# Optimization experiments

Measured on AMD Instinct MI355X. Metric: run time of the kernel, lower is better.

The kernel has to match this reference:

```python
import math
import jax, jax.numpy as jnp
import numpy as np

# static config (mirrors init_kwargs / input_specs)
B, HRV, WRV, CRV = 2, 32, 1024, 64
CB, HB, WB = 256, 200, 200
D, COUT, HEADS, POINTS = 128, 128, 8, 6
DH = D // HEADS
RMAX = 55.0
XMIN, XMAX, YMIN, YMAX = -50.0, 50.0, -50.0, 50.0


def group_norm(x, gamma, beta, groups, eps=1e-5):
    b, h, w, c = x.shape
    xg = x.reshape(b, h, w, groups, c // groups)
    mean = xg.mean(axis=(1, 2, 4), keepdims=True)
    var = xg.var(axis=(1, 2, 4), keepdims=True)
    xg = (xg - mean) * jax.lax.rsqrt(var + eps)
    return xg.reshape(b, h, w, c) * gamma + beta


def fwd(x_rv, bev, pq_w, pq_b, pv_w, pv_b, po_w, po_b, qs_w1, qs_b1, qs_w2, qs_b2,
        rh_w1, rh_b1, rh_g1, rh_be1, rh_w2, rh_g2, rh_be2, rh_w3, rh_b3,
        so_w, so_b, aw_w, aw_b, vp_w, vp_b, op_w, op_b):
    b = x_rv.shape[0]
    nq = HRV * WRV
    az = jnp.linspace(-math.pi, math.pi, WRV + 1)[:-1]  # [Wrv]
    az = jnp.broadcast_to(az[None, None, :], (b, HRV, WRV))
    coord = jnp.stack([jnp.sin(az), jnp.cos(az), jnp.zeros_like(az)], axis=-1)  # [b,H,W,3]
    Q0 = x_rv @ pq_w + pq_b                                  # 1x1 conv as matmul (NHWC)
    Vmap = bev.transpose(0, 2, 3, 1) @ pv_w + pv_b           # [b,HB,WB,D]
    # range head: 1x1 conv -> GN(8) -> GELU -> 3x3 circular conv -> GN(8) -> GELU -> 1x1 conv
    h = jnp.concatenate([x_rv, coord], axis=-1) @ rh_w1 + rh_b1
    h = jax.nn.gelu(group_norm(h, rh_g1, rh_be1, 8), approximate=False)
    hp = jnp.pad(h, ((0, 0), (1, 1), (1, 1), (0, 0)), mode='wrap')  # circular padding
    h = jax.lax.conv_general_dilated(hp, rh_w2, (1, 1), 'VALID',
                                     dimension_numbers=('NHWC', 'HWIO', 'NHWC'))
    h = jax.nn.gelu(group_norm(h, rh_g2, rh_be2, 8), approximate=False)
    rh = h @ rh_w3 + rh_b3                                   # [b,H,W,2]
    mu = jnp.clip(rh[..., 0], 0.0, RMAX)                     # [b,H,W]
    log_sigma = jnp.clip(rh[..., 1:2], -5.0, 3.0)            # [b,H,W,1]
    sigma = jnp.exp(log_sigma)
    x_mu = mu * jnp.cos(az)
    y_mu = mu * jnp.sin(az)
    rx = jnp.clip((x_mu - XMIN) / (XMAX - XMIN), 0.0, 1.0)
    ry = jnp.clip((y_mu - YMIN) / (YMAX - YMIN), 0.0, 1.0)
    ref = jnp.stack([rx, ry], axis=-1).reshape(b, nq, 2)
    sig_feat = jnp.concatenate([log_sigma, 1.0 / (sigma + 1e-6)], axis=-1)
    q = jnp.concatenate([Q0, sig_feat], axis=-1) @ qs_w1 + qs_b1
    q = jax.nn.gelu(q, approximate=False) @ qs_w2 + qs_b2
    query = q.reshape(b, nq, D)
    # ---- MSDA (num_levels = 1) ----
    value = Vmap.reshape(b, HB * WB, D) @ vp_w + vp_b
    vflat = value.reshape(b, HB * WB, HEADS, DH).transpose(0, 2, 1, 3)  # [b,heads,NV,dh]
    offs = (query @ so_w + so_b).reshape(b, nq, HEADS, POINTS, 2)
    attw = jax.nn.softmax((query @ aw_w + aw_b).reshape(b, nq, HEADS, POINTS), axis=-1)
    norm = jnp.array([WB, HB], dtype=query.dtype)            # offset_normalizer = [W, H]
    loc = ref[:, :, None, None, :] + offs / norm             # [b,nq,heads,P,2] in [0,1]
    loc = loc.transpose(0, 2, 1, 3, 4)                       # [b,heads,nq,P,2]
    attw = attw.transpose(0, 2, 1, 3)                        # [b,heads,nq,P]
    # grid_sample bilinear, zero padding, align_corners=False: pix = loc*size - 0.5
    px = loc[..., 0] * WB - 0.5
    py = loc[..., 1] * HB - 0.5
    x0 = jnp.floor(px).astype(jnp.int32)
    y0 = jnp.floor(py).astype(jnp.int32)
    wx = px - x0
    wy = py - y0

    def gather(xi, yi):
        valid = (xi >= 0) & (xi < WB) & (yi >= 0) & (yi < HB)
        idx = jnp.clip(yi, 0, HB - 1) * WB + jnp.clip(xi, 0, WB - 1)
        g = jnp.take_along_axis(vflat, idx.reshape(b, HEADS, nq * POINTS, 1), axis=2)
        return g.reshape(b, HEADS, nq, POINTS, DH) * valid[..., None]

    sampled = (gather(x0, y0) * ((1 - wx) * (1 - wy))[..., None]
               + gather(x0 + 1, y0) * (wx * (1 - wy))[..., None]
               + gather(x0, y0 + 1) * ((1 - wx) * wy)[..., None]
               + gather(x0 + 1, y0 + 1) * (wx * wy)[..., None])    # [b,heads,nq,P,dh]
    out = (sampled * attw[..., None]).sum(axis=3)                  # [b,heads,nq,dh]
    out = out.transpose(0, 2, 1, 3).reshape(b, nq, D) @ op_w + op_b
    y = out.reshape(b, HRV, WRV, D) @ po_w + po_b                  # proj_o (1x1 conv)
    return y                                                       # [b,Hrv,Wrv,C_out]


def setup_inputs() -> dict:
    key = jax.random.key(0)
    ks = jax.random.split(key, 20)
    def rn(i, shape, s=0.02):
        return s * jax.random.normal(ks[i], shape, jnp.float32)
    z = lambda n: jnp.zeros((n,), jnp.float32)
    o = lambda n: jnp.ones((n,), jnp.float32)
    return dict(
        x_rv=rn(0, (B, HRV, WRV, CRV), 1.0),
        bev=rn(1, (B, CB, HB, WB), 1.0),
        pq_w=rn(2, (CRV, D)), pq_b=z(D),
        pv_w=rn(3, (CB, D)), pv_b=z(D),
        po_w=rn(4, (D, COUT)), po_b=z(COUT),
        qs_w1=rn(5, (D + 2, D)), qs_b1=z(D),
        qs_w2=rn(6, (D, D)), qs_b2=z(D),
        rh_w1=rn(7, (CRV + 3, 128)), rh_b1=z(128),
        rh_g1=o(128), rh_be1=z(128),
        rh_w2=rn(8, (3, 3, 128, 64)),
        rh_g2=o(64), rh_be2=z(64),
        rh_w3=rn(9, (64, 2)), rh_b3=z(2),
        so_w=rn(10, (D, HEADS * POINTS * 2)), so_b=rn(11, (HEADS * POINTS * 2,), 0.5),
        aw_w=rn(12, (D, HEADS * POINTS)), aw_b=z(HEADS * POINTS),
        vp_w=rn(13, (D, D)), vp_b=z(D),
        op_w=rn(14, (D, D)), op_b=z(D),
    )


def reference(x_rv, bev, pq_w, pq_b, pv_w, pv_b, po_w, po_b, qs_w1, qs_b1, qs_w2, qs_b2,
              rh_w1, rh_b1, rh_g1, rh_be1, rh_w2, rh_g2, rh_be2, rh_w3, rh_b3,
              so_w, so_b, aw_w, aw_b, vp_w, vp_b, op_w, op_b):
    return fwd(x_rv, bev, pq_w, pq_b, pv_w, pv_b, po_w, po_b, qs_w1, qs_b1, qs_w2, qs_b2,
               rh_w1, rh_b1, rh_g1, rh_be1, rh_w2, rh_g2, rh_be2, rh_w3, rh_b3,
               so_w, so_b, aw_w, aw_b, vp_w, vp_b, op_w, op_b)
```

## Files before the change

### kernel.cpp

```cpp
#include <hip/hip_runtime.h>
#include <math.h>

#define PI_F 3.14159265358979323846f


typedef __attribute__((ext_vector_type(8))) short bf16x8;
typedef __attribute__((ext_vector_type(4))) float f32x4;

__device__ __forceinline__ float gelu_f(float x) {
    return 0.5f * x * (1.0f + erff(x * 0.70710678118654752440f));
}

__device__ __forceinline__ unsigned short f2bf(float x) {
    unsigned int u = __float_as_uint(x);
    u += 0x7fffu + ((u >> 16) & 1u);
    return (unsigned short)(u >> 16);
}

__device__ __forceinline__ float bf2f(unsigned short h) {
    return __uint_as_float((unsigned int)h << 16);
}

__global__ void prep_weights(const float* __restrict__ pv_w, const float* __restrict__ pv_b,
                             const float* __restrict__ vp_w, const float* __restrict__ vp_b,
                             const float* __restrict__ op_w, const float* __restrict__ op_b,
                             const float* __restrict__ po_w, const float* __restrict__ po_b,
                             const float* __restrict__ pq_w, const float* __restrict__ pq_b,
                             const float* __restrict__ qs_w1, const float* __restrict__ qs_b1,
                             const float* __restrict__ qs_w2, const float* __restrict__ qs_b2,
                             const float* __restrict__ so_w, const float* __restrict__ so_b,
                             const float* __restrict__ aw_w, const float* __restrict__ aw_b,
                             const float* __restrict__ rh_w2,
                             unsigned short* __restrict__ wvh, unsigned short* __restrict__ wvl,
                             float* __restrict__ pvvp_b,
                             float* __restrict__ oppo_w, float* __restrict__ oppo_b,
                             float* __restrict__ pqqs_w, float* __restrict__ pqqs_b,
                             float* __restrict__ qsso_w, float* __restrict__ qsso_b,
                             float* __restrict__ qsaw_w, float* __restrict__ qsaw_b,
                             unsigned short* __restrict__ wtb,
                             float2* __restrict__ azsc) {
    int r = blockIdx.x;
    int d = threadIdx.x;
    if (r < 256) {
        float s = 0.f;
        for (int k = 0; k < 128; ++k) s += pv_w[r * 128 + k] * vp_w[k * 128 + d];
        unsigned short h = f2bf(s);
        wvh[d * 256 + r] = h;
        wvl[d * 256 + r] = f2bf(s - bf2f(h));
    } else if (r == 256) {
        float s = vp_b[d];
        for (int k = 0; k < 128; ++k) s += pv_b[k] * vp_w[k * 128 + d];
        pvvp_b[d] = s;
    } else if (r < 385) {
        int rr = r - 257;
        float s = 0.f;
        for (int k = 0; k < 128; ++k) s += op_w[rr * 128 + k] * po_w[k * 128 + d];
        oppo_w[rr * 128 + d] = s;
    } else if (r == 385) {
        float s = po_b[d];
        for (int k = 0; k < 128; ++k) s += op_b[k] * po_w[k * 128 + d];
        oppo_b[d] = s;
    } else if (r < 450) {
        int rr = r - 386;
        float s = 0.f;
        for (int k = 0; k < 128; ++k) s += pq_w[rr * 128 + k] * qs_w1[k * 128 + d];
        pqqs_w[rr * 128 + d] = s;
    } else if (r == 450) {
        float s = qs_b1[d];
        for (int k = 0; k < 128; ++k) s += pq_b[k] * qs_w1[k * 128 + d];
        pqqs_b[d] = s;
    } else if (r < 459) {
        int w = (r - 451) * 128 + d;
        float az = -PI_F + (float)w * (6.283185307179586f / 1024.0f);
        azsc[w] = make_float2(sinf(az), cosf(az));
    } else if (r < 587) {
        int rr = r - 459;
        if (d < 96) {
            float s = 0.f;
            for (int k = 0; k < 128; ++k) s += qs_w2[rr * 128 + k] * so_w[k * 96 + d];
            qsso_w[rr * 96 + d] = s;
        }
    } else if (r == 587) {
        if (d < 96) {
            float s = so_b[d];
            for (int k = 0; k < 128; ++k) s += qs_b2[k] * so_w[k * 96 + d];
            qsso_b[d] = s;
        }
    } else if (r < 716) {
        int rr = r - 588;
        if (d < 48) {
            float s = 0.f;
            for (int k = 0; k < 128; ++k) s += qs_w2[rr * 128 + k] * aw_w[k * 48 + d];
            qsaw_w[rr * 48 + d] = s;
        }
    } else if (r == 716) {
        if (d < 48) {
            float s = aw_b[d];
            for (int k = 0; k < 128; ++k) s += qs_b2[k] * aw_w[k * 48 + d];
            qsaw_b[d] = s;
        }
    } else {
        int idx = (r - 717) * 128 + d;
        int ci = idx & 31;
        int o = (idx >> 5) & 63;
        int cc4i = (idx >> 11) & 3;
        int tap = idx >> 13;
        float w = rh_w2[((size_t)tap * 128 + cc4i * 32 + ci) * 64 + o];
        wtb[idx] = f2bf(w);
    }
}

template <int NT, bool STATS>
__global__ __launch_bounds__(2 * NT) void gemm_v3(
    const float* __restrict__ A, int lda,
    const float* __restrict__ W,
    const float* __restrict__ bias,
    float* __restrict__ C, int K,
    const float2* __restrict__ azsc,
    const float* __restrict__ extra2,
    const float* __restrict__ extra_w,
    int emode, int do_gelu, float* __restrict__ stats1) {
    constexpr int NTH = 2 * NT;
    constexpr int NTO = NT / 8;
    __shared__ float As[32][140];
    __shared__ float Ws[32][NT];
    __shared__ float sred[8][2];
    const int tid = threadIdx.x;
    const int tn = tid % NTO;
    const int tm = tid / NTO;
    const int m0 = blockIdx.x * 128;
    if (STATS && tid < 16) sred[tid >> 1][tid & 1] = 0.f;
    float acc[8][8];
#pragma unroll
    for (int i = 0; i < 8; ++i)
#pragma unroll
        for (int j = 0; j < 8; ++j) acc[i][j] = 0.f;

    for (int k0 = 0; k0 < K; k0 += 32) {
        __syncthreads();
        for (int f = tid; f < 1024; f += NTH) {
            int r = f >> 3, c4 = f & 7;
            float4 v = *(const float4*)(A + (size_t)(m0 + r) * lda + k0 + c4 * 4);
            As[c4 * 4 + 0][r] = v.x;
            As[c4 * 4 + 1][r] = v.y;
            As[c4 * 4 + 2][r] = v.z;
            As[c4 * 4 + 3][r] = v.w;
        }
        for (int f = tid; f < 8 * NT; f += NTH) {
            int kk = f / (NT / 4), n4 = f % (NT / 4);
            *(float4*)&Ws[kk][n4 * 4] = *(const float4*)(W + (size_t)(k0 + kk) * NT + n4 * 4);
        }
        __syncthreads();
#pragma unroll 2
        for (int k = 0; k < 32; ++k) {
            const float4 a0 = *(const float4*)&As[k][tm * 8];
            const float4 a1 = *(const float4*)&As[k][tm * 8 + 4];
            const float4 w0 = *(const float4*)&Ws[k][tn * 8];
            const float4 w1 = *(const float4*)&Ws[k][tn * 8 + 4];
            const float av[8] = {a0.x, a0.y, a0.z, a0.w, a1.x, a1.y, a1.z, a1.w};
            const float wv[8] = {w0.x, w0.y, w0.z, w0.w, w1.x, w1.y, w1.z, w1.w};
#pragma unroll
            for (int i = 0; i < 8; ++i)
#pragma unroll
                for (int j = 0; j < 8; ++j) acc[i][j] += av[i] * wv[j];
        }
    }
    float bv[8], e0w[8], e1w[8];
#pragma unroll
    for (int j = 0; j < 8; ++j) bv[j] = bias[tn * 8 + j];
    if (emode) {
#pragma unroll
        for (int j = 0; j < 8; ++j) {
            e0w[j] = extra_w[tn * 8 + j];
            e1w[j] = extra_w[NT + tn * 8 + j];
        }
    }
    float ts = 0.f, ts2 = 0.f;
#pragma unroll
    for (int i = 0; i < 8; ++i) {
        int m = m0 + tm * 8 + i;
        float e0 = 0.f, e1 = 0.f;
        if (emode == 1) {
            float2 sc = azsc[m & 1023];
            e0 = sc.x; e1 = sc.y;
        } else if (emode == 2) {
            e0 = extra2[2 * (size_t)m];
            e1 = extra2[2 * (size_t)m + 1];
        }
        float o[8];
#pragma unroll
        for (int j = 0; j < 8; ++j) {
            float v = acc[i][j] + bv[j];
            if (emode) v += e0 * e0w[j] + e1 * e1w[j];
            if (do_gelu) v = gelu_f(v);
            if (STATS) { ts += v; ts2 += v * v; }
            o[j] = v;
        }
        *(float4*)(C + (size_t)m * NT + tn * 8) = make_float4(o[0], o[1], o[2], o[3]);
        *(float4*)(C + (size_t)m * NT + tn * 8 + 4) = make_float4(o[4], o[5], o[6], o[7]);
    }
    if (STATS) {
        atomicAdd(&sred[tn >> 1][0], ts);
        atomicAdd(&sred[tn >> 1][1], ts2);
        __syncthreads();
        if (tid < 8) {
            int b = m0 >> 15;
            atomicAdd(&stats1[(b * 8 + tid) * 2 + 0], sred[tid][0]);
            atomicAdd(&stats1[(b * 8 + tid) * 2 + 1], sred[tid][1]);
        }
    }
}

template <int MT, int NT, int NTH>
__global__ __launch_bounds__(NTH) void gemm_rn(
    const float* __restrict__ A, int lda,
    const float* __restrict__ W, int ldw,
    const float* __restrict__ bias,
    float* __restrict__ C, int ldc, int K) {
    static_assert(NTH == (MT / 8) * (NT / 4), "thread count mismatch");
    __shared__ float As[32][MT + 12];
    __shared__ float Ws[32][NT];
    constexpr int NTN = NT / 4;
    const int tid = threadIdx.x;
    const int tn = tid % NTN;
    const int tm = tid / NTN;
    const int m0 = blockIdx.x * MT;
    float acc[8][4];
#pragma unroll
    for (int i = 0; i < 8; ++i)
#pragma unroll
        for (int j = 0; j < 4; ++j) acc[i][j] = 0.f;

    for (int k0 = 0; k0 < K; k0 += 32) {
        __syncthreads();
        for (int f = tid; f < MT * 8; f += NTH) {
            int r = f >> 3, c4 = f & 7;
            float4 v = *(const float4*)(A + (size_t)(m0 + r) * lda + k0 + c4 * 4);
            As[c4 * 4 + 0][r] = v.x;
            As[c4 * 4 + 1][r] = v.y;
            As[c4 * 4 + 2][r] = v.z;
            As[c4 * 4 + 3][r] = v.w;
        }
        for (int f = tid; f < 8 * NT; f += NTH) {
            int kk = f / NTN, n4 = f % NTN;
            *(float4*)&Ws[kk][n4 * 4] = *(const float4*)(W + (size_t)(k0 + kk) * ldw + n4 * 4);
        }
        __syncthreads();
#pragma unroll 4
        for (int k = 0; k < 32; ++k) {
            const float4 a0 = *(const float4*)&As[k][tm * 8];
            const float4 a1 = *(const float4*)&As[k][tm * 8 + 4];
            const float4 wv = *(const float4*)&Ws[k][tn * 4];
            acc[0][0] += a0.x * wv.x; acc[0][1] += a0.x * wv.y; acc[0][2] += a0.x * wv.z; acc[0][3] += a0.x * wv.w;
            acc[1][0] += a0.y * wv.x; acc[1][1] += a0.y * wv.y; acc[1][2] += a0.y * wv.z; acc[1][3] += a0.y * wv.w;
            acc[2][0] += a0.z * wv.x; acc[2][1] += a0.z * wv.y; acc[2][2] += a0.z * wv.z; acc[2][3] += a0.z * wv.w;
            acc[3][0] += a0.w * wv.x; acc[3][1] += a0.w * wv.y; acc[3][2] += a0.w * wv.z; acc[3][3] += a0.w * wv.w;
            acc[4][0] += a1.x * wv.x; acc[4][1] += a1.x * wv.y; acc[4][2] += a1.x * wv.z; acc[4][3] += a1.x * wv.w;
            acc[5][0] += a1.y * wv.x; acc[5][1] += a1.y * wv.y; acc[5][2] += a1.y * wv.z; acc[5][3] += a1.y * wv.w;
            acc[6][0] += a1.z * wv.x; acc[6][1] += a1.z * wv.y; acc[6][2] += a1.z * wv.z; acc[6][3] += a1.z * wv.w;
            acc[7][0] += a1.w * wv.x; acc[7][1] += a1.w * wv.y; acc[7][2] += a1.w * wv.z; acc[7][3] += a1.w * wv.w;
        }
    }
#pragma unroll
    for (int i = 0; i < 8; ++i) {
        int m = m0 + tm * 8 + i;
        float4 o;
        o.x = acc[i][0] + bias[tn * 4 + 0];
        o.y = acc[i][1] + bias[tn * 4 + 1];
        o.z = acc[i][2] + bias[tn * 4 + 2];
        o.w = acc[i][3] + bias[tn * 4 + 3];
        *(float4*)(C + (size_t)m * ldc + tn * 4) = o;
    }
}

__global__ __launch_bounds__(256) void value_gemm_mfma(
    const float* __restrict__ bev,
    const unsigned short* __restrict__ Wh, const unsigned short* __restrict__ Wl,
    const float* __restrict__ bf, float* __restrict__ V) {
    __shared__ __align__(16) short Ah0_s[64 * 40];
    __shared__ __align__(16) short Al0_s[64 * 40];
    __shared__ __align__(16) short Ah1_s[64 * 40];
    __shared__ __align__(16) short Al1_s[64 * 40];
    const int tid = threadIdx.x;
    const int wid = tid >> 6;
    const int lane = tid & 63;
    const int m = lane & 15;
    const int quad = lane >> 4;
    const int n0 = blockIdx.x * 64;
    const int b = blockIdx.y;
    const int wr = (wid >> 1) * 32;
    const int wc = (wid & 1) * 64;
    f32x4 acc[2][4];
#pragma unroll
    for (int i = 0; i < 2; ++i)
#pragma unroll
        for (int j = 0; j < 4; ++j) acc[i][j] = (f32x4){0.f, 0.f, 0.f, 0.f};

    const int sn = tid & 63;
    const int kq = tid >> 6;
    const float* srcA = bev + (size_t)b * 256 * 40000 + n0 + sn;
    const unsigned short* pBh[4];
    const unsigned short* pBl[4];
#pragma unroll
    for (int j = 0; j < 4; ++j) {
        size_t off = (size_t)(wc + j * 16 + m) * 256 + quad * 8;
        pBh[j] = Wh + off;
        pBl[j] = Wl + off;
    }

    float va[8];
    bf16x8 vbh[4], vbl[4];
#pragma unroll
    for (int j = 0; j < 8; ++j) va[j] = srcA[(size_t)(kq * 8 + j) * 40000];
#pragma unroll
    for (int j = 0; j < 4; ++j) {
        vbh[j] = *(const bf16x8*)(pBh[j]);
        vbl[j] = *(const bf16x8*)(pBl[j]);
    }

    short* pAh = Ah0_s; short* pAl = Al0_s;
    short* qAh = Ah1_s; short* qAl = Al1_s;

    for (int t = 0; t < 8; ++t) {
        const int k0 = t * 32;
        uint4 ph, pl;
        {
            unsigned hp[4], lp[4];
#pragma unroll
            for (int pj = 0; pj < 4; ++pj) {
                float x0 = va[2 * pj], x1 = va[2 * pj + 1];
                unsigned u0 = __float_as_uint(x0), u1 = __float_as_uint(x1);
                hp[pj] = __builtin_amdgcn_perm(u1, u0, 0x07060302);
                float h0 = __uint_as_float(u0 & 0xffff0000u);
                float h1 = __uint_as_float(u1 & 0xffff0000u);
                float l0 = x0 - h0, l1 = x1 - h1;
                asm("v_cvt_pk_bf16_f32 %0, %1, %2" : "=v"(lp[pj]) : "v"(l0), "v"(l1));
            }
            ph = make_uint4(hp[0], hp[1], hp[2], hp[3]);
            pl = make_uint4(lp[0], lp[1], lp[2], lp[3]);
        }
        *(uint4*)&pAh[sn * 40 + kq * 8] = ph;
        *(uint4*)&pAl[sn * 40 + kq * 8] = pl;
        if (t < 7) {
#pragma unroll
            for (int j = 0; j < 8; ++j)
                va[j] = srcA[(size_t)(k0 + 32 + kq * 8 + j) * 40000];
        }
        asm volatile("s_waitcnt lgkmcnt(0)" ::: "memory");
        __builtin_amdgcn_sched_barrier(0);
        __builtin_amdgcn_s_barrier();
        __builtin_amdgcn_sched_barrier(0);
        bf16x8 ah[2], al[2];
#pragma unroll
        for (int i = 0; i < 2; ++i) {
            ah[i] = *(const bf16x8*)&pAh[(wr + i * 16 + m) * 40 + quad * 8];
            al[i] = *(const bf16x8*)&pAl[(wr + i * 16 + m) * 40 + quad * 8];
        }
#pragma unroll
        for (int i = 0; i < 2; ++i)
#pragma unroll
            for (int j = 0; j < 4; ++j) {
                acc[i][j] = __builtin_amdgcn_mfma_f32_16x16x32_bf16(ah[i], vbh[j], acc[i][j], 0, 0, 0);
                acc[i][j] = __builtin_amdgcn_mfma_f32_16x16x32_bf16(ah[i], vbl[j], acc[i][j], 0, 0, 0);
                acc[i][j] = __builtin_amdgcn_mfma_f32_16x16x32_bf16(al[i], vbh[j], acc[i][j], 0, 0, 0);
            }
        if (t < 7) {
#pragma unroll
            for (int j = 0; j < 4; ++j) {
                vbh[j] = *(const bf16x8*)(pBh[j] + k0 + 32);
                vbl[j] = *(const bf16x8*)(pBl[j] + k0 + 32);
            }
        }
        short* th = pAh; pAh = qAh; qAh = th;
        short* tl = pAl; pAl = qAl; qAl = tl;
    }
    float bv[4];
#pragma unroll
    for (int j = 0; j < 4; ++j) bv[j] = bf[wc + j * 16 + m];
#pragma unroll
    for (int i = 0; i < 2; ++i) {
        int nbase = n0 + wr + i * 16 + quad * 4;
#pragma unroll
        for (int r = 0; r < 4; ++r) {
            int n = nbase + r;
            float* vp = V + ((size_t)b * 40000 + n) * 128 + wc + m;
#pragma unroll
            for (int j = 0; j < 4; ++j) vp[j * 16] = acc[i][j][r] + bv[j];
        }
    }
}

__global__ __launch_bounds__(256) void gn1_bf16(
    const float* __restrict__ X, const float* __restrict__ stats,
    const float* __restrict__ g1, const float* __restrict__ be1,
    unsigned short* __restrict__ Ob) {
    size_t i4 = (size_t)blockIdx.x * 256 + threadIdx.x;
    size_t base = i4 * 4;
    int c = (int)(base & 127);
    int mrow = (int)(base >> 7);
    int b = mrow >> 15;
    int g = c >> 4;
    float mean = stats[(b * 8 + g) * 2 + 0] * (1.0f / 524288.0f);
    float var = stats[(b * 8 + g) * 2 + 1] * (1.0f / 524288.0f) - mean * mean;
    float rs = 1.0f / sqrtf(var + 1e-5f);
    float4 x = *(const float4*)(X + base);
    float4 gm = *(const float4*)(g1 + c);
    float4 bt = *(const float4*)(be1 + c);
    ushort4 o;
    o.x = f2bf(gelu_f((x.x - mean) * rs * gm.x + bt.x));
    o.y = f2bf(gelu_f((x.y - mean) * rs * gm.y + bt.y));
    o.z = f2bf(gelu_f((x.z - mean) * rs * gm.z + bt.z));
    o.w = f2bf(gelu_f((x.w - mean) * rs * gm.w + bt.w));
    *(ushort4*)(Ob + base) = o;
}

__global__ __launch_bounds__(256, 4) void conv3x3_mfma(
    const unsigned short* __restrict__ H1b,
    const unsigned short* __restrict__ Wtb,
    float* __restrict__ Y,
    float* __restrict__ stats2) {
    __shared__ short As_s[66 * 40];
    __shared__ short Ws_s[3 * 64 * 40];
    __shared__ float sred[8][2];
    const int tid = threadIdx.x;
    const int wid = tid >> 6;
    const int lane = tid & 63;
    const int m = lane & 15;
    const int quad = lane >> 4;
    const int x0 = blockIdx.x * 64;
    const int y = blockIdx.y;
    const int b = blockIdx.z;
    if (tid < 16) sred[tid >> 1][tid & 1] = 0.f;
    f32x4 acc[4];
#pragma unroll
    for (int oq = 0; oq < 4; ++oq) acc[oq] = (f32x4){0.f, 0.f, 0.f, 0.f};

    const unsigned short* Hb = H1b + (size_t)b * 32 * 1024 * 128;
    for (int ry = 0; ry < 3; ++ry) {
        const int gy = (y + ry + 31) & 31;
        const unsigned short* Hrow = Hb + (size_t)gy * 1024 * 128;
        for (int cc4 = 0; cc4 < 4; ++cc4) {
            __syncthreads();
            for (int f = tid; f < 264; f += 256) {
                int xx = f >> 2, cq = f & 3;
                int gx = (x0 + xx + 1023) & 1023;
                uint4 v = *(const uint4*)(Hrow + (size_t)gx * 128 + cc4 * 32 + cq * 8);
                *(uint4*)&As_s[xx * 40 + cq * 8] = v;
            }
            for (int f = tid; f < 768; f += 256) {
                int cq = f & 3, o = (f >> 2) & 63, dx = f >> 8;
                int tap = ry * 3 + dx;
                uint4 v = *(const uint4*)(Wtb + ((size_t)(tap * 4 + cc4) * 64 + o) * 32 + cq * 8);
                *(uint4*)&Ws_s[(dx * 64 + o) * 40 + cq * 8] = v;
            }
            __syncthreads();
            const int arow = wid * 16 + m;
#pragma unroll
            for (int dx = 0; dx < 3; ++dx) {
                bf16x8 a = *(const bf16x8*)&As_s[(arow + dx) * 40 + quad * 8];
#pragma unroll
                for (int oq = 0; oq < 4; ++oq) {
                    bf16x8 bfr = *(const bf16x8*)&Ws_s[(dx * 64 + oq * 16 + m) * 40 + quad * 8];
                    acc[oq] = __builtin_amdgcn_mfma_f32_16x16x32_bf16(a, bfr, acc[oq], 0, 0, 0);
                }
            }
        }
    }
    float sv[4], qv[4];
#pragma unroll
    for (int oq = 0; oq < 4; ++oq) {
        sv[oq] = acc[oq].x + acc[oq].y + acc[oq].z + acc[oq].w;
        qv[oq] = acc[oq].x * acc[oq].x + acc[oq].y * acc[oq].y +
                 acc[oq].z * acc[oq].z + acc[oq].w * acc[oq].w;
    }
    const int masks[5] = {1, 2, 4, 16, 32};
#pragma unroll
    for (int mi = 0; mi < 5; ++mi) {
#pragma unroll
        for (int oq = 0; oq < 4; ++oq) {
            sv[oq] += __shfl_xor(sv[oq], masks[mi]);
            qv[oq] += __shfl_xor(qv[oq], masks[mi]);
        }
    }
    if ((lane & 55) == 0) {
        int gb = (lane >> 3) & 1;
#pragma unroll
        for (int oq = 0; oq < 4; ++oq) {
            atomicAdd(&sred[oq * 2 + gb][0], sv[oq]);
            atomicAdd(&sred[oq * 2 + gb][1], qv[oq]);
        }
    }
    const int pxb = x0 + wid * 16 + quad * 4;
    float* Yb = Y + ((size_t)(b * 32 + y) * 1024 + pxb) * 64;
#pragma unroll
    for (int oq = 0; oq < 4; ++oq) {
        const float av[4] = {acc[oq].x, acc[oq].y, acc[oq].z, acc[oq].w};
#pragma unroll
        for (int r = 0; r < 4; ++r) Yb[(size_t)r * 64 + oq * 16 + m] = av[r];
    }
    __syncthreads();
    if (tid < 16)
        atomicAdd(&stats2[(b * 8 + (tid >> 1)) * 2 + (tid & 1)], sred[tid >> 1][tid & 1]);
}

__global__ __launch_bounds__(256) void rh3_kernel(
    const float* __restrict__ H2, const float* __restrict__ stats,
    const float* __restrict__ gamma, const float* __restrict__ beta, float inv_cnt,
    const float* __restrict__ w3, const float* __restrict__ b3,
    const float2* __restrict__ azsc,
    float2* __restrict__ refxy, float2* __restrict__ sigf) {
    const int tid = threadIdx.x;
    const int lane = tid & 15;
    const int m = blockIdx.x * 16 + (tid >> 4);
    const int b = m >> 15;
    const int c = lane * 4;
    const int g = c >> 3;
    float mean = stats[(b * 8 + g) * 2 + 0] * inv_cnt;
    float var = stats[(b * 8 + g) * 2 + 1] * inv_cnt - mean * mean;
    float rs = 1.0f / sqrtf(var + 1e-5f);
    float4 v = *(const float4*)(H2 + (size_t)m * 64 + c);
    float hv[4];
    hv[0] = gelu_f((v.x - mean) * rs * gamma[c + 0] + beta[c + 0]);
    hv[1] = gelu_f((v.y - mean) * rs * gamma[c + 1] + beta[c + 1]);
    hv[2] = gelu_f((v.z - mean) * rs * gamma[c + 2] + beta[c + 2]);
    hv[3] = gelu_f((v.w - mean) * rs * gamma[c + 3] + beta[c + 3]);
    float d0 = 0.f, d1 = 0.f;
#pragma unroll
    for (int k = 0; k < 4; ++k) {
        d0 += hv[k] * w3[(c + k) * 2 + 0];
        d1 += hv[k] * w3[(c + k) * 2 + 1];
    }
#pragma unroll
    for (int s = 1; s < 16; s <<= 1) {
        d0 += __shfl_xor(d0, s, 16);
        d1 += __shfl_xor(d1, s, 16);
    }
    if (lane == 0) {
        float mu = fminf(fmaxf(d0 + b3[0], 0.f), 55.f);
        float ls = fminf(fmaxf(d1 + b3[1], -5.f), 3.f);
        float sg = expf(ls);
        float2 sc = azsc[m & 1023];
        float rx = fminf(fmaxf(mu * sc.y * 0.01f + 0.5f, 0.f), 1.f);
        float ry = fminf(fmaxf(mu * sc.x * 0.01f + 0.5f, 0.f), 1.f);
        refxy[m] = make_float2(rx, ry);
        sigf[m] = make_float2(ls, 1.f / (sg + 1e-6f));
    }
}

__global__ __launch_bounds__(256) void msda_kernel(
    const float* __restrict__ V, const float2* __restrict__ refxy,
    const float* __restrict__ offs, const float* __restrict__ aw,
    float* __restrict__ out) {
    const int tid = threadIdx.x;
    const int l4 = tid & 3;
    const int grp = tid >> 2;
    const int m = blockIdx.x * 8 + (grp >> 3);
    const int head = grp & 7;
    const int b = m >> 15;
    float2 r = refxy[m];
    const float* lg = aw + (size_t)m * 48 + head * 6;
    float l[6];
#pragma unroll
    for (int p = 0; p < 6; ++p) l[p] = lg[p];
    float mx = l[0];
#pragma unroll
    for (int p = 1; p < 6; ++p) mx = fmaxf(mx, l[p]);
    float s = 0.f;
#pragma unroll
    for (int p = 0; p < 6; ++p) { l[p] = expf(l[p] - mx); s += l[p]; }
    float inv = 1.f / s;
#pragma unroll
    for (int p = 0; p < 6; ++p) l[p] *= inv;
    const float* of = offs + (size_t)m * 96 + head * 12;
    const float* Vb = V + (size_t)b * 40000 * 128 + head * 16 + l4 * 4;
    const float bx = r.x * 200.f - 0.5f;
    const float by = r.y * 200.f - 0.5f;
    f32x4 acc = (f32x4){0.f, 0.f, 0.f, 0.f};
#pragma unroll
    for (int p = 0; p < 6; ++p) {
        float px = bx + of[p * 2 + 0];
        float py = by + of[p * 2 + 1];
        float fx = floorf(px), fy = floorf(py);
        int x0 = (int)fx, y0 = (int)fy;
        float wx = px - fx, wy = py - fy;
        int xc0 = min(max(x0, 0), 199), xc1 = min(max(x0 + 1, 0), 199);
        int yc0 = min(max(y0, 0), 199), yc1 = min(max(y0 + 1, 0), 199);
        bool vx0 = ((unsigned)x0 < 200u), vx1 = ((unsigned)(x0 + 1) < 200u);
        bool vy0 = ((unsigned)y0 < 200u), vy1 = ((unsigned)(y0 + 1) < 200u);
        const f32x4 v00 = *(const f32x4*)(Vb + ((size_t)(yc0 * 200 + xc0)) * 128);
        const f32x4 v10 = *(const f32x4*)(Vb + ((size_t)(yc0 * 200 + xc1)) * 128);
        const f32x4 v01 = *(const f32x4*)(Vb + ((size_t)(yc1 * 200 + xc0)) * 128);
        const f32x4 v11 = *(const f32x4*)(Vb + ((size_t)(yc1 * 200 + xc1)) * 128);
        float w = l[p];
        float w00 = (vx0 && vy0) ? w * (1.f - wx) * (1.f - wy) : 0.f;
        float w10 = (vx1 && vy0) ? w * wx * (1.f - wy) : 0.f;
        float w01 = (vx0 && vy1) ? w * (1.f - wx) * wy : 0.f;
        float w11 = (vx1 && vy1) ? w * wx * wy : 0.f;
        acc += v00 * w00;
        acc += v10 * w10;
        acc += v01 * w01;
        acc += v11 * w11;
    }
    *(f32x4*)(out + (size_t)m * 128 + head * 16 + l4 * 4) = acc;
}

extern "C" void kernel_launch(void* const* d_in, const int* in_sizes, int n_in,
                              void* d_out, int out_size, void* d_ws, size_t ws_size,
                              hipStream_t stream) {
    const float* x_rv = (const float*)d_in[0];
    const float* bev = (const float*)d_in[1];
    const float* pq_w = (const float*)d_in[2];
    const float* pq_b = (const float*)d_in[3];
    const float* pv_w = (const float*)d_in[4];
    const float* pv_b = (const float*)d_in[5];
    const float* po_w = (const float*)d_in[6];
    const float* po_b = (const float*)d_in[7];
    const float* qs_w1 = (const float*)d_in[8];
    const float* qs_b1 = (const float*)d_in[9];
    const float* qs_w2 = (const float*)d_in[10];
    const float* qs_b2 = (const float*)d_in[11];
    const float* rh_w1 = (const float*)d_in[12];
    const float* rh_b1 = (const float*)d_in[13];
    const float* rh_g1 = (const float*)d_in[14];
    const float* rh_be1 = (const float*)d_in[15];
    const float* rh_w2 = (const float*)d_in[16];
    const float* rh_g2 = (const float*)d_in[17];
    const float* rh_be2 = (const float*)d_in[18];
    const float* rh_w3 = (const float*)d_in[19];
    const float* rh_b3 = (const float*)d_in[20];
    const float* so_w = (const float*)d_in[21];
    const float* so_b = (const float*)d_in[22];
    const float* aw_w = (const float*)d_in[23];
    const float* aw_b = (const float*)d_in[24];
    const float* vp_w = (const float*)d_in[25];
    const float* vp_b = (const float*)d_in[26];
    const float* op_w = (const float*)d_in[27];
    const float* op_b = (const float*)d_in[28];

    const int M = 65536;

    float* ws = (float*)d_ws;
    float* azsc = ws;    ws += 2048;
    unsigned short* wvh = (unsigned short*)ws; ws += 16384;
    unsigned short* wvl = (unsigned short*)ws; ws += 16384;
    float* pvvp_b = ws;  ws += 128;
    float* oppo_w = ws;  ws += 128 * 128;
    float* oppo_b = ws;  ws += 128;
    float* pqqs_w = ws;  ws += 64 * 128;
    float* pqqs_b = ws;  ws += 128;
    float* qsso_w = ws;  ws += 128 * 96;
    float* qsso_b = ws;  ws += 128;
    float* qsaw_w = ws;  ws += 128 * 48;
    float* qsaw_b = ws;  ws += 64;
    float* stats = ws;   ws += 64;
    unsigned short* wtb = (unsigned short*)ws;  ws += 36864;
    unsigned short* h1b = (unsigned short*)ws;  ws += (size_t)M * 64;
    float* Vv = ws;      ws += (size_t)80000 * 128;
    float* h1 = ws;      ws += (size_t)M * 128;
    float* h2 = ws;      ws += (size_t)M * 64;
    float* q1 = ws;      ws += (size_t)M * 128;
    float* refxy = ws;   ws += (size_t)M * 2;
    float* sigf = ws;    ws += (size_t)M * 2;
    size_t need_bytes = (size_t)(ws - (float*)d_ws) * sizeof(float);
    if (ws_size < need_bytes) return;
    float* offs = h1;
    float* attw = h2;
    float* mo = q1;

    float2* azsc2 = (float2*)azsc;
    float2* refxy2 = (float2*)refxy;
    float2* sigf2 = (float2*)sigf;

    prep_weights<<<1293, 128, 0, stream>>>(
        pv_w, pv_b, vp_w, vp_b, op_w, op_b, po_w, po_b, pq_w, pq_b,
        qs_w1, qs_b1, qs_w2, qs_b2, so_w, so_b, aw_w, aw_b, rh_w2,
        wvh, wvl, pvvp_b, oppo_w, oppo_b, pqqs_w, pqqs_b,
        qsso_w, qsso_b, qsaw_w, qsaw_b, wtb, azsc2);
    hipMemsetAsync(stats, 0, 64 * sizeof(float), stream);

    gemm_v3<128, true><<<M / 128, 256, 0, stream>>>(
        x_rv, 64, rh_w1, rh_b1, h1, 64, azsc2, nullptr, rh_w1 + 64 * 128, 1, 0, stats);

    value_gemm_mfma<<<dim3(625, 2), 256, 0, stream>>>(bev, wvh, wvl, pvvp_b, Vv);

    gn1_bf16<<<8192, 256, 0, stream>>>(h1, stats, rh_g1, rh_be1, h1b);

    conv3x3_mfma<<<dim3(16, 32, 2), 256, 0, stream>>>(h1b, wtb, h2, stats + 32);

    rh3_kernel<<<4096, 256, 0, stream>>>(h2, stats + 32, rh_g2, rh_be2, 1.0f / 262144.0f,
                                         rh_w3, rh_b3, azsc2, refxy2, sigf2);

    gemm_v3<128, false><<<M / 128, 256, 0, stream>>>(
        x_rv, 64, pqqs_w, pqqs_b, q1, 64, nullptr, sigf, qs_w1 + 128 * 128, 2, 1, nullptr);

    gemm_v3<96, false><<<M / 128, 192, 0, stream>>>(
        q1, 128, qsso_w, qsso_b, offs, 128, nullptr, nullptr, nullptr, 0, 0, nullptr);

    gemm_rn<128, 48, 192><<<M / 128, 192, 0, stream>>>(
        q1, 128, qsaw_w, 48, qsaw_b, attw, 48, 128);

    msda_kernel<<<M / 8, 256, 0, stream>>>(Vv, refxy2, offs, attw, mo);

    gemm_v3<128, false><<<M / 128, 256, 0, stream>>>(
        mo, 128, oppo_w, oppo_b, (float*)d_out, 128, nullptr, nullptr, nullptr, 0, 0, nullptr);
}
```

Baseline: 486.2 us.

## Restructure BEV value GEMM with float4 staging and pre-swizzled weight layout

The value-projection GEMM now stages raw fp32 BEV tiles in LDS with coalesced float4 global loads and does the bf16 hi/lo split at fragment-read time, replacing per-thread strided scalar loads. Weights are pre-swizzled in prep_weights so each lane reads its MFMA B fragment contiguously, and these fragments are loaded directly from global memory every K step. Blocks grow to 512 threads covering 128 pixels, with a clamped tail and guarded stores. The kernel is also launched before the range-head GEMM. In exchange there are more LDS reads and conversions per wave, and weight loads are no longer prefetched one step ahead.

Result: faster. 469.6 us (-3.4%).

```diff
diff --git a/kernel.cpp b/kernel.cpp
--- a/kernel.cpp
+++ b/kernel.cpp
@@ -45,8 +45,11 @@
         float s = 0.f;
         for (int k = 0; k < 128; ++k) s += pv_w[r * 128 + k] * vp_w[k * 128 + d];
         unsigned short h = f2bf(s);
-        wvh[d * 256 + r] = h;
-        wvl[d * 256 + r] = f2bf(s - bf2f(h));
+        int dt = d >> 4, mm = d & 15;
+        int kc = r >> 5, qd = (r >> 3) & 3, jj = r & 7;
+        size_t off = (((size_t)(dt * 8 + kc) * 64) + qd * 16 + mm) * 8 + jj;
+        wvh[off] = h;
+        wvl[off] = f2bf(s - bf2f(h));
     } else if (r == 256) {
         float s = vp_b[d];
         for (int k = 0; k < 128; ++k) s += pv_b[k] * vp_w[k * 128 + d];
@@ -273,119 +276,141 @@
     }
 }
 
-__global__ __launch_bounds__(256) void value_gemm_mfma(
+__global__ __launch_bounds__(512) void value_gemm_fused(
     const float* __restrict__ bev,
     const unsigned short* __restrict__ Wh, const unsigned short* __restrict__ Wl,
     const float* __restrict__ bf, float* __restrict__ V) {
-    __shared__ __align__(16) short Ah0_s[64 * 40];
-    __shared__ __align__(16) short Al0_s[64 * 40];
-    __shared__ __align__(16) short Ah1_s[64 * 40];
-    __shared__ __align__(16) short Al1_s[64 * 40];
+    __shared__ __align__(16) float T0[32 * 134];
+    __shared__ __align__(16) float T1[32 * 134];
     const int tid = threadIdx.x;
     const int wid = tid >> 6;
     const int lane = tid & 63;
     const int m = lane & 15;
     const int quad = lane >> 4;
-    const int n0 = blockIdx.x * 64;
+    const int n0 = blockIdx.x * 128;
     const int b = blockIdx.y;
-    const int wr = (wid >> 1) * 32;
-    const int wc = (wid & 1) * 64;
+    const int wn = wid >> 1;
+    const int wd = wid & 1;
+    const float* src = bev + (size_t)b * 256 * 40000;
+
+    int srow[2];
+    const float* sp[2];
+    int lcol[2];
+#pragma unroll
+    for (int i = 0; i < 2; ++i) {
+        int f = tid + i * 512;
+        srow[i] = f >> 5;
+        lcol[i] = (f & 31) * 4;
+        int nl = n0 + lcol[i];
+        if (nl > 39996) nl = 39996;
+        sp[i] = src + nl;
+    }
+
     f32x4 acc[2][4];
 #pragma unroll
     for (int i = 0; i < 2; ++i)
 #pragma unroll
         for (int j = 0; j < 4; ++j) acc[i][j] = (f32x4){0.f, 0.f, 0.f, 0.f};
 
-    const int sn = tid & 63;
-    const int kq = tid >> 6;
-    const float* srcA = bev + (size_t)b * 256 * 40000 + n0 + sn;
-    const unsigned short* pBh[4];
-    const unsigned short* pBl[4];
-#pragma unroll
-    for (int j = 0; j < 4; ++j) {
-        size_t off = (size_t)(wc + j * 16 + m) * 256 + quad * 8;
-        pBh[j] = Wh + off;
-        pBl[j] = Wl + off;
-    }
-
-    float va[8];
-    bf16x8 vbh[4], vbl[4];
-#pragma unroll
-    for (int j = 0; j < 8; ++j) va[j] = srcA[(size_t)(kq * 8 + j) * 40000];
-#pragma unroll
-    for (int j = 0; j < 4; ++j) {
-        vbh[j] = *(const bf16x8*)(pBh[j]);
-        vbl[j] = *(const bf16x8*)(pBl[j]);
-    }
-
-    short* pAh = Ah0_s; short* pAl = Al0_s;
-    short* qAh = Ah1_s; short* qAl = Al1_s;
+    const int dt0 = wd * 4;
+    size_t bb[4];
+#pragma unroll
+    for (int j = 0; j < 4; ++j) bb[j] = (size_t)(dt0 + j) * 4096 + lane * 8;
+
+    union UV { uint4 u; bf16x8 v; };
+    float4 st[2];
+
+#define LOADG(K0)                                                           \
+    {                                                                       \
+        _Pragma("unroll")                                                   \
+        for (int i_ = 0; i_ < 2; ++i_)                                      \
+            st[i_] = *(const float4*)(sp[i_] + (size_t)((K0) + srow[i_]) * 40000); \
+    }
+#define WRITELDS(TB)                                                        \
+    {                                                                       \
+        _Pragma("unroll")                                                   \
+        for (int i_ = 0; i_ < 2; ++i_) {                                    \
+            float* d_ = (TB) + srow[i_] * 134 + lcol[i_];                   \
+            *(float2*)(d_ + 0) = make_float2(st[i_].x, st[i_].y);           \
+            *(float2*)(d_ + 2) = make_float2(st[i_].z, st[i_].w);           \
+        }                                                                   \
+    }
+
+    float* Tc = T0;
+    float* Tn = T1;
+    LOADG(0);
+    WRITELDS(Tc);
+    LOADG(32);
+    asm volatile("s_waitcnt lgkmcnt(0)" ::: "memory");
+    __builtin_amdgcn_sched_barrier(0);
+    __builtin_amdgcn_s_barrier();
+    __builtin_amdgcn_sched_barrier(0);
 
     for (int t = 0; t < 8; ++t) {
-        const int k0 = t * 32;
-        uint4 ph, pl;
-        {
-            unsigned hp[4], lp[4];
-#pragma unroll
-            for (int pj = 0; pj < 4; ++pj) {
-                float x0 = va[2 * pj], x1 = va[2 * pj + 1];
-                unsigned u0 = __float_as_uint(x0), u1 = __float_as_uint(x1);
-                hp[pj] = __builtin_amdgcn_perm(u1, u0, 0x07060302);
-                float h0 = __uint_as_float(u0 & 0xffff0000u);
-                float h1 = __uint_as_float(u1 & 0xffff0000u);
-                float l0 = x0 - h0, l1 = x1 - h1;
-                asm("v_cvt_pk_bf16_f32 %0, %1, %2" : "=v"(lp[pj]) : "v"(l0), "v"(l1));
+        bf16x8 ah[2], al[2];
+#pragma unroll
+        for (int i = 0; i < 2; ++i) {
+            const int nc = wn * 32 + i * 16 + m;
+            float f8[8];
+#pragma unroll
+            for (int jj = 0; jj < 8; ++jj)
+                f8[jj] = Tc[(quad * 8 + jj) * 134 + nc];
+            unsigned hh[4], ll[4];
+#pragma unroll
+            for (int q = 0; q < 4; ++q) {
+                unsigned u0 = __float_as_uint(f8[2 * q]);
+                unsigned u1 = __float_as_uint(f8[2 * q + 1]);
+                hh[q] = __builtin_amdgcn_perm(u1, u0, 0x07060302);
+                float l0 = f8[2 * q] - __uint_as_float(u0 & 0xffff0000u);
+                float l1 = f8[2 * q + 1] - __uint_as_float(u1 & 0xffff0000u);
+                asm("v_cvt_pk_bf16_f32 %0, %1, %2" : "=v"(ll[q]) : "v"(l0), "v"(l1));
             }
-            ph = make_uint4(hp[0], hp[1], hp[2], hp[3]);
-            pl = make_uint4(lp[0], lp[1], lp[2], lp[3]);
-        }
-        *(uint4*)&pAh[sn * 40 + kq * 8] = ph;
-        *(uint4*)&pAl[sn * 40 + kq * 8] = pl;
-        if (t < 7) {
-#pragma unroll
-            for (int j = 0; j < 8; ++j)
-                va[j] = srcA[(size_t)(k0 + 32 + kq * 8 + j) * 40000];
-        }
-        asm volatile("s_waitcnt lgkmcnt(0)" ::: "memory");
-        __builtin_amdgcn_sched_barrier(0);
-        __builtin_amdgcn_s_barrier();
-        __builtin_amdgcn_sched_barrier(0);
-        bf16x8 ah[2], al[2];
-#pragma unroll
-        for (int i = 0; i < 2; ++i) {
-            ah[i] = *(const bf16x8*)&pAh[(wr + i * 16 + m) * 40 + quad * 8];
-            al[i] = *(const bf16x8*)&pAl[(wr + i * 16 + m) * 40 + quad * 8];
+            UV th, tl;
+            th.u = make_uint4(hh[0], hh[1], hh[2], hh[3]);
+            tl.u = make_uint4(ll[0], ll[1], ll[2], ll[3]);
+            ah[i] = th.v;
+            al[i] = tl.v;
+        }
+        if (t < 7) WRITELDS(Tn);
+        if (t < 6) LOADG(t * 32 + 64);
+        bf16x8 bh[4], bl[4];
+#pragma unroll
+        for (int j = 0; j < 4; ++j) {
+            bh[j] = *(const bf16x8*)(Wh + bb[j] + t * 512);
+            bl[j] = *(const bf16x8*)(Wl + bb[j] + t * 512);
         }
 #pragma unroll
         for (int i = 0; i < 2; ++i)
 #pragma unroll
             for (int j = 0; j < 4; ++j) {
-                acc[i][j] = __builtin_amdgcn_mfma_f32_16x16x32_bf16(ah[i], vbh[j], acc[i][j], 0, 0, 0);
-                acc[i][j] = __builtin_amdgcn_mfma_f32_16x16x32_bf16(ah[i], vbl[j], acc[i][j], 0, 0, 0);
-                acc[i][j] = __builtin_amdgcn_mfma_f32_16x16x32_bf16(al[i], vbh[j], acc[i][j], 0, 0, 0);
+                acc[i][j] = __builtin_amdgcn_mfma_f32_16x16x32_bf16(ah[i], bh[j], acc[i][j], 0, 0, 0);
+                acc[i][j] = __builtin_amdgcn_mfma_f32_16x16x32_bf16(ah[i], bl[j], acc[i][j], 0, 0, 0);
+                acc[i][j] = __builtin_amdgcn_mfma_f32_16x16x32_bf16(al[i], bh[j], acc[i][j], 0, 0, 0);
             }
         if (t < 7) {
-#pragma unroll
-            for (int j = 0; j < 4; ++j) {
-                vbh[j] = *(const bf16x8*)(pBh[j] + k0 + 32);
-                vbl[j] = *(const bf16x8*)(pBl[j] + k0 + 32);
-            }
-        }
-        short* th = pAh; pAh = qAh; qAh = th;
-        short* tl = pAl; pAl = qAl; qAl = tl;
-    }
+            asm volatile("s_waitcnt lgkmcnt(0)" ::: "memory");
+            __builtin_amdgcn_sched_barrier(0);
+            __builtin_amdgcn_s_barrier();
+            __builtin_amdgcn_sched_barrier(0);
+            float* tmp = Tc; Tc = Tn; Tn = tmp;
+        }
+    }
+#undef LOADG
+#undef WRITELDS
     float bv[4];
 #pragma unroll
-    for (int j = 0; j < 4; ++j) bv[j] = bf[wc + j * 16 + m];
+    for (int j = 0; j < 4; ++j) bv[j] = bf[wd * 64 + j * 16 + m];
 #pragma unroll
     for (int i = 0; i < 2; ++i) {
-        int nbase = n0 + wr + i * 16 + quad * 4;
+        int nbase = n0 + wn * 32 + i * 16 + quad * 4;
 #pragma unroll
         for (int r = 0; r < 4; ++r) {
             int n = nbase + r;
-            float* vp = V + ((size_t)b * 40000 + n) * 128 + wc + m;
-#pragma unroll
-            for (int j = 0; j < 4; ++j) vp[j * 16] = acc[i][j][r] + bv[j];
+            if (n < 40000) {
+                float* vp = V + ((size_t)b * 40000 + n) * 128 + wd * 64 + m;
+#pragma unroll
+                for (int j = 0; j < 4; ++j) vp[j * 16] = acc[i][j][r] + bv[j];
+            }
         }
     }
 }
@@ -678,11 +703,11 @@
         qsso_w, qsso_b, qsaw_w, qsaw_b, wtb, azsc2);
     hipMemsetAsync(stats, 0, 64 * sizeof(float), stream);
 
+    value_gemm_fused<<<dim3(313, 2), 512, 0, stream>>>(bev, wvh, wvl, pvvp_b, Vv);
+
     gemm_v3<128, true><<<M / 128, 256, 0, stream>>>(
         x_rv, 64, rh_w1, rh_b1, h1, 64, azsc2, nullptr, rh_w1 + 64 * 128, 1, 0, stats);
 
-    value_gemm_mfma<<<dim3(625, 2), 256, 0, stream>>>(bev, wvh, wvl, pvvp_b, Vv);
-
     gn1_bf16<<<8192, 256, 0, stream>>>(h1, stats, rh_g1, rh_be1, h1b);
 
     conv3x3_mfma<<<dim3(16, 32, 2), 256, 0, stream>>>(h1b, wtb, h2, stats + 32);
```
